# Kernel optimization log

Measured on AMD Instinct MI355X. Metric: run time of the kernel, lower is better.

## Reference

```python
import jax, jax.numpy as jnp
import numpy as np

NEG_BIG = -9.0e15  # matches torch's -9000000000000000.0 mask fill
ALPHA = 0.2        # LeakyReLU negative slope


def setup_inputs() -> dict:
    key = jax.random.key(0)
    k1, k2, k3, k4 = jax.random.split(key, 4)
    bs, N, F_in, F_out = 4, 4096, 512, 64
    x = jax.random.normal(k1, (bs, N, F_in), dtype=jnp.float32)
    adj = jax.random.randint(k2, (N, N), 0, 2, dtype=jnp.int32)
    # xavier_uniform with gain=1.414
    lim_W = 1.414 * np.sqrt(6.0 / (F_in + F_out))
    W = jax.random.uniform(k3, (F_in, F_out), minval=-lim_W, maxval=lim_W, dtype=jnp.float32)
    lim_a = 1.414 * np.sqrt(6.0 / (2 * F_out + 1))
    a = jax.random.uniform(k4, (2 * F_out, 1), minval=-lim_a, maxval=lim_a, dtype=jnp.float32)
    return {"x": x, "adj": adj, "W": W, "a": a}


def reference(x, adj, W, a):
    # h = x @ W : [bs, N, F_out]
    h = jnp.einsum('bnf,fo->bno', x, W)
    F_out = W.shape[1]
    a1, a2 = a[:F_out, 0], a[F_out:, 0]  # each [F_out]
    # e_ij = LeakyReLU(a1.Wh_i + a2.Wh_j) -- same math as the O(N^2*2F) concat
    s1 = jnp.einsum('bno,o->bn', h, a1)  # [bs, N]
    s2 = jnp.einsum('bno,o->bn', h, a2)  # [bs, N]
    e = s1[:, :, None] + s2[:, None, :]  # [bs, N, N]
    e = jax.nn.leaky_relu(e, negative_slope=ALPHA)
    mask = (adj > 0)[None, :, :]
    attention = jnp.where(mask, e, NEG_BIG)
    attention = jax.nn.softmax(attention, axis=-1)
    # dropout is identity in eval mode (p applied only during training)
    h_prime = jnp.einsum('bij,bjo->bio', attention, h)
    return jax.nn.elu(h_prime)  # concat=True path
```

## Files before the change

### kernel.cpp

```cpp
#include <hip/hip_runtime.h>

#define LOG2E 1.4426950408889634f

typedef __attribute__((ext_vector_type(8))) short short8;
typedef __attribute__((ext_vector_type(4))) float f32x4;
using u32 = unsigned int;
using u16 = unsigned short;
using u64 = unsigned long long;

__global__ __launch_bounds__(256) void prep_kernel(const int* __restrict__ adj,
                                                   u32* __restrict__ mask_t,
                                                   const float* __restrict__ W,
                                                   u16* __restrict__ wt) {
    if (blockIdx.x >= 2048) {
        int t = (blockIdx.x - 2048) * 256 + threadIdx.x;
        int n = t >> 7, k4 = (t & 127) << 2;
        u32 c0 = __float_as_uint(W[(size_t)(k4 + 0) * 64 + n]) + 0x8000u;
        u32 c1 = __float_as_uint(W[(size_t)(k4 + 1) * 64 + n]) + 0x8000u;
        u32 c2 = __float_as_uint(W[(size_t)(k4 + 2) * 64 + n]) + 0x8000u;
        u32 c3 = __float_as_uint(W[(size_t)(k4 + 3) * 64 + n]) + 0x8000u;
        uint2 o;
        o.x = (c0 >> 16) | (c1 & 0xffff0000u);
        o.y = (c2 >> 16) | (c3 & 0xffff0000u);
        *(uint2*)(wt + (size_t)n * 512 + k4) = o;
        return;
    }
    const int wid = (blockIdx.x * 256 + threadIdx.x) >> 6;
    const int lane = threadIdx.x & 63;
    for (int t = wid; t < 65536; t += 8192) {
        const int r = t >> 4, c4 = t & 15;
        const int* base = adj + (size_t)r * 4096 + c4 * 256 + lane;
        int v0 = __builtin_nontemporal_load(base);
        int v1 = __builtin_nontemporal_load(base + 64);
        int v2 = __builtin_nontemporal_load(base + 128);
        int v3 = __builtin_nontemporal_load(base + 192);
        u64 b0 = __ballot(v0 > 0);
        u64 b1 = __ballot(v1 > 0);
        u64 b2 = __ballot(v2 > 0);
        u64 b3 = __ballot(v3 > 0);
        if (lane < 8) {
            u64 bv = (lane & 4) ? ((lane & 2) ? b3 : b2) : ((lane & 2) ? b1 : b0);
            u32 w = (u32)(bv >> ((lane & 1) << 5));
            mask_t[(size_t)(c4 * 8 + lane) * 4096 + r] = w;
        }
    }
}

__global__ __launch_bounds__(512) void k1f(const float* __restrict__ x,
                                           const u16* __restrict__ wt,
                                           const float* __restrict__ a,
                                           u16* __restrict__ h_t,
                                           float* __restrict__ s1p,
                                           float* __restrict__ s2p) {
    __shared__ float red[4][16][65];
    const int rt = blockIdx.x, b = blockIdx.y;
    const int tid = threadIdx.x, wave = tid >> 6, lane = tid & 63;
    const int g = wave & 3, kz = wave >> 2;
    const int m = lane & 15, quad = lane >> 4;
    const int row = rt * 64 + g * 16 + m;
    const float* xb = x + ((size_t)b * 4096 + row) * 512 + kz * 256 + quad * 8;
    const u16* wb = wt + (size_t)m * 512 + kz * 256 + quad * 8;

    f32x4 acc[4];
#pragma unroll
    for (int ot = 0; ot < 4; ot++) acc[ot] = (f32x4){0.f, 0.f, 0.f, 0.f};

    union BU { uint4 q; short8 v; };
    float4 ax[2][2];
    BU bw[2][4];
#pragma unroll
    for (int s = 0; s < 2; s++) {
        ax[s][0] = *(const float4*)(xb + s * 32);
        ax[s][1] = *(const float4*)(xb + s * 32 + 4);
#pragma unroll
        for (int ot = 0; ot < 4; ot++)
            bw[s][ot].q = *(const uint4*)(wb + (size_t)ot * 16 * 512 + s * 32);
    }
#pragma unroll
    for (int s = 0; s < 8; s++) {
        const int cur = s & 1;
        union { u32 u[4]; short8 v; } af;
        const float* a0 = (const float*)&ax[cur][0];
#pragma unroll
        for (int p = 0; p < 4; p++) {
            u32 lo = __float_as_uint(a0[2 * p]) + 0x8000u;
            u32 hi = __float_as_uint(a0[2 * p + 1]) + 0x8000u;
            af.u[p] = __builtin_amdgcn_perm(hi, lo, 0x07060302u);
        }
#pragma unroll
        for (int ot = 0; ot < 4; ot++)
            acc[ot] = __builtin_amdgcn_mfma_f32_16x16x32_bf16(af.v, bw[cur][ot].v,
                                                              acc[ot], 0, 0, 0);
        if (s + 2 < 8) {
            ax[cur][0] = *(const float4*)(xb + (s + 2) * 32);
            ax[cur][1] = *(const float4*)(xb + (s + 2) * 32 + 4);
#pragma unroll
            for (int ot = 0; ot < 4; ot++)
                bw[cur][ot].q =
                    *(const uint4*)(wb + (size_t)ot * 16 * 512 + (s + 2) * 32);
        }
    }
    if (kz) {
#pragma unroll
        for (int ot = 0; ot < 4; ot++)
#pragma unroll
            for (int r = 0; r < 4; r++)
                red[g][quad * 4 + r][ot * 16 + m] = acc[ot][r];
    }
    __syncthreads();
    if (kz) return;
#pragma unroll
    for (int ot = 0; ot < 4; ot++)
#pragma unroll
        for (int r = 0; r < 4; r++)
            acc[ot][r] += red[g][quad * 4 + r][ot * 16 + m];

    float a1v[4], a2v[4];
#pragma unroll
    for (int ot = 0; ot < 4; ot++) {
        a1v[ot] = a[ot * 16 + m];
        a2v[ot] = a[64 + ot * 16 + m];
    }
    float s1r[4], s2r[4];
#pragma unroll
    for (int r = 0; r < 4; r++) {
        s1r[r] = 0.f; s2r[r] = 0.f;
#pragma unroll
        for (int ot = 0; ot < 4; ot++) {
            s1r[r] = fmaf(acc[ot][r], a1v[ot], s1r[r]);
            s2r[r] = fmaf(acc[ot][r], a2v[ot], s2r[r]);
        }
    }
#pragma unroll
    for (int d = 1; d < 16; d <<= 1) {
#pragma unroll
        for (int r = 0; r < 4; r++) {
            s1r[r] += __shfl_xor(s1r[r], d);
            s2r[r] += __shfl_xor(s2r[r], d);
        }
    }
    if (m == 0) {
#pragma unroll
        for (int r = 0; r < 4; r++) {
            int rr = rt * 64 + g * 16 + quad * 4 + r;
            s1p[b * 4096 + rr] = s1r[r] * LOG2E;
            s2p[b * 4096 + rr] = s2r[r] * LOG2E;
        }
    }
#pragma unroll
    for (int ot = 0; ot < 4; ot++) {
        u32 b0 = __float_as_uint(acc[ot][0]) + 0x8000u;
        u32 b1 = __float_as_uint(acc[ot][1]) + 0x8000u;
        u32 b2 = __float_as_uint(acc[ot][2]) + 0x8000u;
        u32 b3 = __float_as_uint(acc[ot][3]) + 0x8000u;
        uint2 u;
        u.x = (b0 >> 16) | (b1 & 0xffff0000u);
        u.y = (b2 >> 16) | (b3 & 0xffff0000u);
        *(uint2*)(h_t + ((size_t)(b * 64 + ot * 16 + m)) * 4096
                  + rt * 64 + g * 16 + quad * 4) = u;
    }
}

template <int NSTEP>
__global__ __launch_bounds__(256, 8) void k2_attn(const u16* __restrict__ h_t,
                                                  const u32* __restrict__ mask_t,
                                                  const float* __restrict__ s1p,
                                                  const float* __restrict__ s2p,
                                                  u16* __restrict__ part,
                                                  float* __restrict__ lp) {
    constexpr int JSEG = NSTEP * 32;
    constexpr int T = NSTEP / 2;
    __shared__ u16 hB[2][64 * 64];
    __shared__ float s2l[JSEG];
    const int b = blockIdx.y, seg = blockIdx.z, rb = blockIdx.x;
    const int tid = threadIdx.x, wave = tid >> 6, lane = tid & 63;
    const int m = lane & 15, quad = lane >> 4;
    const int row = rb * 64 + wave * 16 + m;
    const int jstart = seg * JSEG;
    const float t1 = s1p[b * 4096 + row];
    const u16* hsrc = h_t + (size_t)b * 64 * 4096 + jstart;
    const u32* mrow = mask_t + (size_t)(jstart >> 5) * 4096 + row;

    for (int t = tid; t < (JSEG >> 2); t += 256)
        ((float4*)s2l)[t] = ((const float4*)(s2p + b * 4096 + jstart))[t];

    f32x4 acc[4], accd;
#pragma unroll
    for (int ot = 0; ot < 4; ot++) acc[ot] = (f32x4){0.f, 0.f, 0.f, 0.f};
    accd = (f32x4){0.f, 0.f, 0.f, 0.f};

    u32 mw[4];
#pragma unroll
    for (int s = 0; s < 4; s++) mw[s] = mrow[(size_t)s * 4096];
    union { u32 u[4]; short8 v; } ones;
#pragma unroll
    for (int p = 0; p < 4; p++) ones.u[p] = 0x3F803F80u;

    const int cj = tid & 7;
    const int ow = tid >> 3;
    uint4 pf[2];
    pf[0] = *(const uint4*)(hsrc + (size_t)ow * 4096 + (cj << 3));
    pf[1] = *(const uint4*)(hsrc + (size_t)(ow + 32) * 4096 + (cj << 3));
    *(uint4*)(hB[0] + (size_t)ow * 64 + ((cj ^ (ow & 7)) << 3)) = pf[0];
    *(uint4*)(hB[0] + (size_t)(ow + 32) * 64 + ((cj ^ ((ow + 32) & 7)) << 3)) = pf[1];
    __syncthreads();

    for (int jt = 0; jt < T; jt++) {
        const int cb = jt & 1;
        if (jt + 1 < T) {
            pf[0] = *(const uint4*)(hsrc + (size_t)ow * 4096 + (jt + 1) * 64 + (cj << 3));
            pf[1] = *(const uint4*)(hsrc + (size_t)(ow + 32) * 4096 + (jt + 1) * 64 + (cj << 3));
        }
#pragma unroll
        for (int ks = 0; ks < 2; ks++) {
            const int s = jt * 2 + ks;
            const u32 mws = mw[s & 3] >> (quad * 8);
            if (s + 4 < NSTEP) mw[(s + 4) & 3] = mrow[(size_t)(s + 4) * 4096];

            const float4 sa = *(const float4*)&s2l[s * 32 + quad * 8];
            const float4 sb = *(const float4*)&s2l[s * 32 + quad * 8 + 4];
            const float sv[8] = {sa.x, sa.y, sa.z, sa.w, sb.x, sb.y, sb.z, sb.w};
            union { u32 u[4]; short8 v; } af;
#pragma unroll
            for (int p = 0; p < 4; p++) {
                float t0 = t1 + sv[2 * p];
                float u0 = fmaxf(t0, 0.2f * t0);
                float w0 = __builtin_amdgcn_exp2f(u0);
                u32 m0 = (u32)(((int)(mws << (31 - 2 * p))) >> 31);
                u32 w0u = __float_as_uint(w0) & m0;
                float t2 = t1 + sv[2 * p + 1];
                float u2 = fmaxf(t2, 0.2f * t2);
                float w1 = __builtin_amdgcn_exp2f(u2);
                u32 m1 = (u32)(((int)(mws << (30 - 2 * p))) >> 31);
                u32 w1u = __float_as_uint(w1) & m1;
                af.u[p] = __builtin_amdgcn_perm(w1u, w0u, 0x07060302u);
            }
            const int jc = ks * 4 + quad;
#pragma unroll
            for (int ot = 0; ot < 4; ot++) {
                const int o = ot * 16 + m;
                short8 bfv = *(const short8*)(hB[cb] + (size_t)o * 64 + ((jc ^ (o & 7)) << 3));
                acc[ot] = __builtin_amdgcn_mfma_f32_16x16x32_bf16(af.v, bfv, acc[ot], 0, 0, 0);
            }
            accd = __builtin_amdgcn_mfma_f32_16x16x32_bf16(af.v, ones.v, accd, 0, 0, 0);
        }
        if (jt + 1 < T) {
            const int nb = cb ^ 1;
            *(uint4*)(hB[nb] + (size_t)ow * 64 + ((cj ^ (ow & 7)) << 3)) = pf[0];
            *(uint4*)(hB[nb] + (size_t)(ow + 32) * 64 + ((cj ^ ((ow + 32) & 7)) << 3)) = pf[1];
        }
        __syncthreads();
    }
    u16* pb = part + (((size_t)(seg * 4 + b) * 4096) + rb * 64 + wave * 16) * 64;
#pragma unroll
    for (int ot = 0; ot < 4; ot++)
#pragma unroll
        for (int r = 0; r < 4; r++) {
            u32 v = __float_as_uint(acc[ot][r]) + 0x8000u;
            pb[(quad * 4 + r) * 64 + ot * 16 + m] = (u16)(v >> 16);
        }
    if (m == 0) {
        float* lpb = lp + (size_t)(seg * 4 + b) * 4096 + rb * 64 + wave * 16 + quad * 4;
#pragma unroll
        for (int r = 0; r < 4; r++) lpb[r] = accd[r];
    }
}

template <int S>
__global__ __launch_bounds__(256) void k3_fin(const u16* __restrict__ part,
                                              const float* __restrict__ lp,
                                              float* __restrict__ out) {
    int idx = blockIdx.x * 256 + threadIdx.x;
    int o4 = (idx & 15) << 2;
    int bi = idx >> 4;
    uint2 pv[S];
    float lv[S];
#pragma unroll
    for (int s = 0; s < S; s++) {
        pv[s] = *(const uint2*)&part[((size_t)s * 16384 + bi) * 64 + o4];
        lv[s] = lp[(size_t)s * 16384 + bi];
    }
    float p0 = 0.f, p1 = 0.f, p2 = 0.f, p3 = 0.f, l = 0.f;
#pragma unroll
    for (int s = 0; s < S; s++) {
        p0 += __uint_as_float(pv[s].x << 16);
        p1 += __uint_as_float(pv[s].x & 0xffff0000u);
        p2 += __uint_as_float(pv[s].y << 16);
        p3 += __uint_as_float(pv[s].y & 0xffff0000u);
        l += lv[s];
    }
    float rl = 1.f / l;
    p0 *= rl; p1 *= rl; p2 *= rl; p3 *= rl;
    float4 o;
    o.x = p0 > 0.f ? p0 : __builtin_amdgcn_exp2f(p0 * LOG2E) - 1.f;
    o.y = p1 > 0.f ? p1 : __builtin_amdgcn_exp2f(p1 * LOG2E) - 1.f;
    o.z = p2 > 0.f ? p2 : __builtin_amdgcn_exp2f(p2 * LOG2E) - 1.f;
    o.w = p3 > 0.f ? p3 : __builtin_amdgcn_exp2f(p3 * LOG2E) - 1.f;
    *(float4*)&out[(size_t)bi * 64 + o4] = o;
}

extern "C" void kernel_launch(void* const* d_in, const int* in_sizes, int n_in,
                              void* d_out, int out_size, void* d_ws, size_t ws_size,
                              hipStream_t stream) {
    const float* x  = (const float*)d_in[0];
    const int* adj  = (const int*)d_in[1];
    const float* W  = (const float*)d_in[2];
    const float* a  = (const float*)d_in[3];
    float* out = (float*)d_out;
    char* ws = (char*)d_ws;

    u16* h_t   = (u16*)ws;
    u32* maskt = (u32*)(ws + (2 << 20));
    float* s1p = (float*)(ws + (4 << 20));
    float* s2p = s1p + 16384;
    float* lp  = s2p + 16384;
    size_t base = (4u << 20) + 2 * 65536;
    int S = 8;
    while (S > 1 && base + (size_t)S * (65536 + 2097152) + 65536 > ws_size) S >>= 1;
    u16* part = (u16*)(ws + base + (size_t)S * 65536);
    u16* wtp = (u16*)(ws + base + (size_t)S * 65536 + (size_t)S * 2097152);

    prep_kernel<<<2080, 256, 0, stream>>>(adj, maskt, W, wtp);
    k1f<<<dim3(64, 4), 512, 0, stream>>>(x, wtp, a, h_t, s1p, s2p);
    if (S == 8)      k2_attn<16><<<dim3(64, 4, 8), 256, 0, stream>>>(h_t, maskt, s1p, s2p, part, lp);
    else if (S == 4) k2_attn<32><<<dim3(64, 4, 4), 256, 0, stream>>>(h_t, maskt, s1p, s2p, part, lp);
    else if (S == 2) k2_attn<64><<<dim3(64, 4, 2), 256, 0, stream>>>(h_t, maskt, s1p, s2p, part, lp);
    else             k2_attn<128><<<dim3(64, 4, 1), 256, 0, stream>>>(h_t, maskt, s1p, s2p, part, lp);
    if (S == 8)      k3_fin<8><<<1024, 256, 0, stream>>>(part, lp, out);
    else if (S == 4) k3_fin<4><<<1024, 256, 0, stream>>>(part, lp, out);
    else if (S == 2) k3_fin<2><<<1024, 256, 0, stream>>>(part, lp, out);
    else             k3_fin<1><<<1024, 256, 0, stream>>>(part, lp, out);
}
```

Baseline: 160.4 us.

## Fuse prep with projection and finalize into attention via last-block counter

Merges the adjacency-mask packing and the x@W projection into one launch. Each projection block converts W to bf16 itself into swizzled shared memory instead of reading a pre-transposed global copy. Removes the separate finalize kernel: the last attention segment block per row tile, found through an atomic counter, reduces the partials and applies normalization and ELU. This cuts three launches to two and drops the W staging buffer. In exchange every projection block redoes the W conversion, the k0 blocks need 64KB of shared memory, and the fused kernel adds threadfences and an atomic.

```diff
diff --git a/kernel.cpp b/kernel.cpp
--- a/kernel.cpp
+++ b/kernel.cpp
@@ -8,73 +8,76 @@
 using u16 = unsigned short;
 using u64 = unsigned long long;
 
-__global__ __launch_bounds__(256) void prep_kernel(const int* __restrict__ adj,
-                                                   u32* __restrict__ mask_t,
-                                                   const float* __restrict__ W,
-                                                   u16* __restrict__ wt) {
-    if (blockIdx.x >= 2048) {
-        int t = (blockIdx.x - 2048) * 256 + threadIdx.x;
-        int n = t >> 7, k4 = (t & 127) << 2;
-        u32 c0 = __float_as_uint(W[(size_t)(k4 + 0) * 64 + n]) + 0x8000u;
-        u32 c1 = __float_as_uint(W[(size_t)(k4 + 1) * 64 + n]) + 0x8000u;
-        u32 c2 = __float_as_uint(W[(size_t)(k4 + 2) * 64 + n]) + 0x8000u;
-        u32 c3 = __float_as_uint(W[(size_t)(k4 + 3) * 64 + n]) + 0x8000u;
-        uint2 o;
-        o.x = (c0 >> 16) | (c1 & 0xffff0000u);
-        o.y = (c2 >> 16) | (c3 & 0xffff0000u);
-        *(uint2*)(wt + (size_t)n * 512 + k4) = o;
+__global__ __launch_bounds__(512) void k0(const int* __restrict__ adj,
+                                          u32* __restrict__ mask_t,
+                                          const float* __restrict__ x,
+                                          const float* __restrict__ W,
+                                          const float* __restrict__ a,
+                                          u16* __restrict__ h_t,
+                                          float* __restrict__ s1p,
+                                          float* __restrict__ s2p,
+                                          u32* __restrict__ cnt) {
+    __shared__ u16 wtl[64 * 512];
+    const int tid = threadIdx.x;
+
+    if (blockIdx.x < 2048) {
+        if (blockIdx.x == 0 && tid < 256) cnt[tid] = 0;
+        const int wid = (blockIdx.x * 512 + tid) >> 6;
+        const int lane = tid & 63;
+        for (int t = wid; t < 65536; t += 16384) {
+            const int r = t >> 4, c4 = t & 15;
+            const int* base = adj + (size_t)r * 4096 + c4 * 256 + lane;
+            int v0 = __builtin_nontemporal_load(base);
+            int v1 = __builtin_nontemporal_load(base + 64);
+            int v2 = __builtin_nontemporal_load(base + 128);
+            int v3 = __builtin_nontemporal_load(base + 192);
+            u64 b0 = __ballot(v0 > 0);
+            u64 b1 = __ballot(v1 > 0);
+            u64 b2 = __ballot(v2 > 0);
+            u64 b3 = __ballot(v3 > 0);
+            if (lane < 8) {
+                u64 bv = (lane & 4) ? ((lane & 2) ? b3 : b2) : ((lane & 2) ? b1 : b0);
+                u32 w = (u32)(bv >> ((lane & 1) << 5));
+                mask_t[(size_t)(c4 * 8 + lane) * 4096 + r] = w;
+            }
+        }
         return;
     }
-    const int wid = (blockIdx.x * 256 + threadIdx.x) >> 6;
-    const int lane = threadIdx.x & 63;
-    for (int t = wid; t < 65536; t += 8192) {
-        const int r = t >> 4, c4 = t & 15;
-        const int* base = adj + (size_t)r * 4096 + c4 * 256 + lane;
-        int v0 = __builtin_nontemporal_load(base);
-        int v1 = __builtin_nontemporal_load(base + 64);
-        int v2 = __builtin_nontemporal_load(base + 128);
-        int v3 = __builtin_nontemporal_load(base + 192);
-        u64 b0 = __ballot(v0 > 0);
-        u64 b1 = __ballot(v1 > 0);
-        u64 b2 = __ballot(v2 > 0);
-        u64 b3 = __ballot(v3 > 0);
-        if (lane < 8) {
-            u64 bv = (lane & 4) ? ((lane & 2) ? b3 : b2) : ((lane & 2) ? b1 : b0);
-            u32 w = (u32)(bv >> ((lane & 1) << 5));
-            mask_t[(size_t)(c4 * 8 + lane) * 4096 + r] = w;
-        }
-    }
-}
-
-__global__ __launch_bounds__(512) void k1f(const float* __restrict__ x,
-                                           const u16* __restrict__ wt,
-                                           const float* __restrict__ a,
-                                           u16* __restrict__ h_t,
-                                           float* __restrict__ s1p,
-                                           float* __restrict__ s2p) {
-    __shared__ float red[4][16][65];
-    const int rt = blockIdx.x, b = blockIdx.y;
-    const int tid = threadIdx.x, wave = tid >> 6, lane = tid & 63;
+    const int bx = blockIdx.x - 2048;
+    const int rt = bx & 63, b = bx >> 6;
+    {
+        const int kk = tid >> 4, n4 = (tid & 15) << 2;
+#pragma unroll
+        for (int it = 0; it < 16; it++) {
+            int k = kk + it * 32;
+            float4 w4 = *(const float4*)(W + (size_t)k * 64 + n4);
+            const float* wf = (const float*)&w4;
+            int kc = k >> 3, ko = k & 7;
+#pragma unroll
+            for (int i = 0; i < 4; i++) {
+                int n = n4 + i;
+                u32 v = __float_as_uint(wf[i]) + 0x8000u;
+                wtl[n * 512 + ((kc ^ (n & 7)) << 3) + ko] = (u16)(v >> 16);
+            }
+        }
+    }
+    __syncthreads();
+
+    const int wave = tid >> 6, lane = tid & 63;
     const int g = wave & 3, kz = wave >> 2;
     const int m = lane & 15, quad = lane >> 4;
     const int row = rt * 64 + g * 16 + m;
     const float* xb = x + ((size_t)b * 4096 + row) * 512 + kz * 256 + quad * 8;
-    const u16* wb = wt + (size_t)m * 512 + kz * 256 + quad * 8;
 
     f32x4 acc[4];
 #pragma unroll
     for (int ot = 0; ot < 4; ot++) acc[ot] = (f32x4){0.f, 0.f, 0.f, 0.f};
 
-    union BU { uint4 q; short8 v; };
     float4 ax[2][2];
-    BU bw[2][4];
 #pragma unroll
     for (int s = 0; s < 2; s++) {
         ax[s][0] = *(const float4*)(xb + s * 32);
         ax[s][1] = *(const float4*)(xb + s * 32 + 4);
-#pragma unroll
-        for (int ot = 0; ot < 4; ot++)
-            bw[s][ot].q = *(const uint4*)(wb + (size_t)ot * 16 * 512 + s * 32);
     }
 #pragma unroll
     for (int s = 0; s < 8; s++) {
@@ -88,24 +91,25 @@
             af.u[p] = __builtin_amdgcn_perm(hi, lo, 0x07060302u);
         }
 #pragma unroll
-        for (int ot = 0; ot < 4; ot++)
-            acc[ot] = __builtin_amdgcn_mfma_f32_16x16x32_bf16(af.v, bw[cur][ot].v,
-                                                              acc[ot], 0, 0, 0);
+        for (int ot = 0; ot < 4; ot++) {
+            const int n = ot * 16 + m;
+            const int chunk = kz * 32 + s * 4 + quad;
+            short8 bv = *(const short8*)(wtl + n * 512 + ((chunk ^ (n & 7)) << 3));
+            acc[ot] = __builtin_amdgcn_mfma_f32_16x16x32_bf16(af.v, bv, acc[ot], 0, 0, 0);
+        }
         if (s + 2 < 8) {
             ax[cur][0] = *(const float4*)(xb + (s + 2) * 32);
             ax[cur][1] = *(const float4*)(xb + (s + 2) * 32 + 4);
-#pragma unroll
-            for (int ot = 0; ot < 4; ot++)
-                bw[cur][ot].q =
-                    *(const uint4*)(wb + (size_t)ot * 16 * 512 + (s + 2) * 32);
-        }
-    }
+        }
+    }
+    __syncthreads();
+    float* red = (float*)wtl;
     if (kz) {
 #pragma unroll
         for (int ot = 0; ot < 4; ot++)
 #pragma unroll
             for (int r = 0; r < 4; r++)
-                red[g][quad * 4 + r][ot * 16 + m] = acc[ot][r];
+                red[(g * 16 + quad * 4 + r) * 64 + ot * 16 + m] = acc[ot][r];
     }
     __syncthreads();
     if (kz) return;
@@ -113,7 +117,7 @@
     for (int ot = 0; ot < 4; ot++)
 #pragma unroll
         for (int r = 0; r < 4; r++)
-            acc[ot][r] += red[g][quad * 4 + r][ot * 16 + m];
+            acc[ot][r] += red[(g * 16 + quad * 4 + r) * 64 + ot * 16 + m];
 
     float a1v[4], a2v[4];
 #pragma unroll
@@ -167,11 +171,15 @@
                                                   const float* __restrict__ s1p,
                                                   const float* __restrict__ s2p,
                                                   u16* __restrict__ part,
-                                                  float* __restrict__ lp) {
+                                                  float* __restrict__ lp,
+                                                  float* __restrict__ out,
+                                                  u32* __restrict__ cnt) {
     constexpr int JSEG = NSTEP * 32;
+    constexpr int S = 128 / NSTEP;
     constexpr int T = NSTEP / 2;
     __shared__ u16 hB[2][64 * 64];
     __shared__ float s2l[JSEG];
+    __shared__ u32 lastf;
     const int b = blockIdx.y, seg = blockIdx.z, rb = blockIdx.x;
     const int tid = threadIdx.x, wave = tid >> 6, lane = tid & 63;
     const int m = lane & 15, quad = lane >> 4;
@@ -264,39 +272,54 @@
 #pragma unroll
         for (int r = 0; r < 4; r++) lpb[r] = accd[r];
     }
-}
-
-template <int S>
-__global__ __launch_bounds__(256) void k3_fin(const u16* __restrict__ part,
-                                              const float* __restrict__ lp,
-                                              float* __restrict__ out) {
-    int idx = blockIdx.x * 256 + threadIdx.x;
-    int o4 = (idx & 15) << 2;
-    int bi = idx >> 4;
-    uint2 pv[S];
-    float lv[S];
-#pragma unroll
+
+    __threadfence();
+    __syncthreads();
+    if (tid == 0) {
+        u32 old = __hip_atomic_fetch_add(&cnt[b * 64 + rb], 1u,
+                                         __ATOMIC_ACQ_REL, __HIP_MEMORY_SCOPE_AGENT);
+        lastf = (old == S - 1) ? 1u : 0u;
+    }
+    __syncthreads();
+    if (!lastf) return;
+    __threadfence();
+
+    const int frow = tid >> 2, c16 = (tid & 3) << 4;
+    float sums[16];
+#pragma unroll
+    for (int i = 0; i < 16; i++) sums[i] = 0.f;
+    float l = 0.f;
     for (int s = 0; s < S; s++) {
-        pv[s] = *(const uint2*)&part[((size_t)s * 16384 + bi) * 64 + o4];
-        lv[s] = lp[(size_t)s * 16384 + bi];
-    }
-    float p0 = 0.f, p1 = 0.f, p2 = 0.f, p3 = 0.f, l = 0.f;
-#pragma unroll
-    for (int s = 0; s < S; s++) {
-        p0 += __uint_as_float(pv[s].x << 16);
-        p1 += __uint_as_float(pv[s].x & 0xffff0000u);
-        p2 += __uint_as_float(pv[s].y << 16);
-        p3 += __uint_as_float(pv[s].y & 0xffff0000u);
-        l += lv[s];
-    }
-    float rl = 1.f / l;
-    p0 *= rl; p1 *= rl; p2 *= rl; p3 *= rl;
-    float4 o;
-    o.x = p0 > 0.f ? p0 : __builtin_amdgcn_exp2f(p0 * LOG2E) - 1.f;
-    o.y = p1 > 0.f ? p1 : __builtin_amdgcn_exp2f(p1 * LOG2E) - 1.f;
-    o.z = p2 > 0.f ? p2 : __builtin_amdgcn_exp2f(p2 * LOG2E) - 1.f;
-    o.w = p3 > 0.f ? p3 : __builtin_amdgcn_exp2f(p3 * LOG2E) - 1.f;
-    *(float4*)&out[(size_t)bi * 64 + o4] = o;
+        const u16* pp = part + (((size_t)(s * 4 + b) * 4096) + rb * 64 + frow) * 64 + c16;
+        uint4 q0 = *(const uint4*)pp;
+        uint4 q1 = *(const uint4*)(pp + 8);
+        const u32* q = (const u32*)&q0;
+#pragma unroll
+        for (int i = 0; i < 4; i++) {
+            sums[2 * i] += __uint_as_float(q[i] << 16);
+            sums[2 * i + 1] += __uint_as_float(q[i] & 0xffff0000u);
+        }
+        const u32* q2 = (const u32*)&q1;
+#pragma unroll
+        for (int i = 0; i < 4; i++) {
+            sums[8 + 2 * i] += __uint_as_float(q2[i] << 16);
+            sums[9 + 2 * i] += __uint_as_float(q2[i] & 0xffff0000u);
+        }
+        l += lp[(size_t)(s * 4 + b) * 4096 + rb * 64 + frow];
+    }
+    const float rl = 1.f / l;
+    float* ob = out + ((size_t)(b * 4096 + rb * 64 + frow)) * 64 + c16;
+#pragma unroll
+    for (int v4 = 0; v4 < 4; v4++) {
+        float4 o;
+        float* ov = (float*)&o;
+#pragma unroll
+        for (int i = 0; i < 4; i++) {
+            float p = sums[v4 * 4 + i] * rl;
+            ov[i] = p > 0.f ? p : __builtin_amdgcn_exp2f(p * LOG2E) - 1.f;
+        }
+        *(float4*)(ob + v4 * 4) = o;
+    }
 }
 
 extern "C" void kernel_launch(void* const* d_in, const int* in_sizes, int n_in,
@@ -313,21 +336,20 @@
     u32* maskt = (u32*)(ws + (2 << 20));
     float* s1p = (float*)(ws + (4 << 20));
     float* s2p = s1p + 16384;
-    float* lp  = s2p + 16384;
-    size_t base = (4u << 20) + 2 * 65536;
+    u32* cnt   = (u32*)(s2p + 16384);
+    float* lp  = (float*)(ws + (4u << 20) + 2 * 65536 + 1024);
+    size_t base = (4u << 20) + 2 * 65536 + 1024;
     int S = 8;
-    while (S > 1 && base + (size_t)S * (65536 + 2097152) + 65536 > ws_size) S >>= 1;
+    while (S > 1 && base + (size_t)S * (65536 + 2097152) > ws_size) S >>= 1;
     u16* part = (u16*)(ws + base + (size_t)S * 65536);
-    u16* wtp = (u16*)(ws + base + (size_t)S * 65536 + (size_t)S * 2097152);
-
-    prep_kernel<<<2080, 256, 0, stream>>>(adj, maskt, W, wtp);
-    k1f<<<dim3(64, 4), 512, 0, stream>>>(x, wtp, a, h_t, s1p, s2p);
-    if (S == 8)      k2_attn<16><<<dim3(64, 4, 8), 256, 0, stream>>>(h_t, maskt, s1p, s2p, part, lp);
-    else if (S == 4) k2_attn<32><<<dim3(64, 4, 4), 256, 0, stream>>>(h_t, maskt, s1p, s2p, part, lp);
-    else if (S == 2) k2_attn<64><<<dim3(64, 4, 2), 256, 0, stream>>>(h_t, maskt, s1p, s2p, part, lp);
-    else             k2_attn<128><<<dim3(64, 4, 1), 256, 0, stream>>>(h_t, maskt, s1p, s2p, part, lp);
-    if (S == 8)      k3_fin<8><<<1024, 256, 0, stream>>>(part, lp, out);
-    else if (S == 4) k3_fin<4><<<1024, 256, 0, stream>>>(part, lp, out);
-    else if (S == 2) k3_fin<2><<<1024, 256, 0, stream>>>(part, lp, out);
-    else             k3_fin<1><<<1024, 256, 0, stream>>>(part, lp, out);
+
+    k0<<<2304, 512, 0, stream>>>(adj, maskt, x, W, a, h_t, s1p, s2p, cnt);
+    if (S == 8)
+        k2_attn<16><<<dim3(64, 4, 8), 256, 0, stream>>>(h_t, maskt, s1p, s2p, part, lp, out, cnt);
+    else if (S == 4)
+        k2_attn<32><<<dim3(64, 4, 4), 256, 0, stream>>>(h_t, maskt, s1p, s2p, part, lp, out, cnt);
+    else if (S == 2)
+        k2_attn<64><<<dim3(64, 4, 2), 256, 0, stream>>>(h_t, maskt, s1p, s2p, part, lp, out, cnt);
+    else
+        k2_attn<128><<<dim3(64, 4, 1), 256, 0, stream>>>(h_t, maskt, s1p, s2p, part, lp, out, cnt);
 }
```

Result: slower. 484.8 us (+202.3%).

## Fuse mask packing and projection GEMM into one kernel with LDS-staged W

Applied to the files above, without the earlier changes.

Merges the adjacency bit-packing kernel and the x@W projection kernel into a single launch, interleaving projection blocks (every 9th block) among mask-packing blocks so both run concurrently. Each projection block now converts W to bf16 itself into an XOR-swizzled shared-memory tile instead of reading a pre-converted copy from global memory, and the reduction buffer reuses that shared memory. This removes one launch and the serialization between the two phases, but each GEMM block redundantly converts all of W and uses 64KB of LDS, which limits occupancy.

```diff
diff --git a/kernel.cpp b/kernel.cpp
--- a/kernel.cpp
+++ b/kernel.cpp
@@ -8,73 +8,76 @@
 using u16 = unsigned short;
 using u64 = unsigned long long;
 
-__global__ __launch_bounds__(256) void prep_kernel(const int* __restrict__ adj,
-                                                   u32* __restrict__ mask_t,
-                                                   const float* __restrict__ W,
-                                                   u16* __restrict__ wt) {
-    if (blockIdx.x >= 2048) {
-        int t = (blockIdx.x - 2048) * 256 + threadIdx.x;
-        int n = t >> 7, k4 = (t & 127) << 2;
-        u32 c0 = __float_as_uint(W[(size_t)(k4 + 0) * 64 + n]) + 0x8000u;
-        u32 c1 = __float_as_uint(W[(size_t)(k4 + 1) * 64 + n]) + 0x8000u;
-        u32 c2 = __float_as_uint(W[(size_t)(k4 + 2) * 64 + n]) + 0x8000u;
-        u32 c3 = __float_as_uint(W[(size_t)(k4 + 3) * 64 + n]) + 0x8000u;
-        uint2 o;
-        o.x = (c0 >> 16) | (c1 & 0xffff0000u);
-        o.y = (c2 >> 16) | (c3 & 0xffff0000u);
-        *(uint2*)(wt + (size_t)n * 512 + k4) = o;
+__global__ __launch_bounds__(512) void k0(const int* __restrict__ adj,
+                                          u32* __restrict__ mask_t,
+                                          const float* __restrict__ x,
+                                          const float* __restrict__ W,
+                                          const float* __restrict__ a,
+                                          u16* __restrict__ h_t,
+                                          float* __restrict__ s1p,
+                                          float* __restrict__ s2p) {
+    __shared__ u16 wtl[64 * 512];
+    const int tid = threadIdx.x;
+    const int bx = blockIdx.x;
+
+    if (bx % 9 != 0) {
+        const int pidx = bx - 1 - bx / 9;
+        const int wid = (pidx * 512 + tid) >> 6;
+        const int lane = tid & 63;
+        for (int t = wid; t < 65536; t += 16384) {
+            const int r = t >> 4, c4 = t & 15;
+            const int* base = adj + (size_t)r * 4096 + c4 * 256 + lane;
+            int v0 = __builtin_nontemporal_load(base);
+            int v1 = __builtin_nontemporal_load(base + 64);
+            int v2 = __builtin_nontemporal_load(base + 128);
+            int v3 = __builtin_nontemporal_load(base + 192);
+            u64 b0 = __ballot(v0 > 0);
+            u64 b1 = __ballot(v1 > 0);
+            u64 b2 = __ballot(v2 > 0);
+            u64 b3 = __ballot(v3 > 0);
+            if (lane < 8) {
+                u64 bv = (lane & 4) ? ((lane & 2) ? b3 : b2) : ((lane & 2) ? b1 : b0);
+                u32 w = (u32)(bv >> ((lane & 1) << 5));
+                mask_t[(size_t)(c4 * 8 + lane) * 4096 + r] = w;
+            }
+        }
         return;
     }
-    const int wid = (blockIdx.x * 256 + threadIdx.x) >> 6;
-    const int lane = threadIdx.x & 63;
-    for (int t = wid; t < 65536; t += 8192) {
-        const int r = t >> 4, c4 = t & 15;
-        const int* base = adj + (size_t)r * 4096 + c4 * 256 + lane;
-        int v0 = __builtin_nontemporal_load(base);
-        int v1 = __builtin_nontemporal_load(base + 64);
-        int v2 = __builtin_nontemporal_load(base + 128);
-        int v3 = __builtin_nontemporal_load(base + 192);
-        u64 b0 = __ballot(v0 > 0);
-        u64 b1 = __ballot(v1 > 0);
-        u64 b2 = __ballot(v2 > 0);
-        u64 b3 = __ballot(v3 > 0);
-        if (lane < 8) {
-            u64 bv = (lane & 4) ? ((lane & 2) ? b3 : b2) : ((lane & 2) ? b1 : b0);
-            u32 w = (u32)(bv >> ((lane & 1) << 5));
-            mask_t[(size_t)(c4 * 8 + lane) * 4096 + r] = w;
-        }
-    }
-}
-
-__global__ __launch_bounds__(512) void k1f(const float* __restrict__ x,
-                                           const u16* __restrict__ wt,
-                                           const float* __restrict__ a,
-                                           u16* __restrict__ h_t,
-                                           float* __restrict__ s1p,
-                                           float* __restrict__ s2p) {
-    __shared__ float red[4][16][65];
-    const int rt = blockIdx.x, b = blockIdx.y;
-    const int tid = threadIdx.x, wave = tid >> 6, lane = tid & 63;
+    const int kidx = bx / 9;
+    const int rt = kidx & 63, b = kidx >> 6;
+    {
+        const int kk = tid >> 4, n4 = (tid & 15) << 2;
+#pragma unroll
+        for (int it = 0; it < 16; it++) {
+            int k = kk + it * 32;
+            float4 w4 = *(const float4*)(W + (size_t)k * 64 + n4);
+            const float* wf = (const float*)&w4;
+            int kc = k >> 3, ko = k & 7;
+#pragma unroll
+            for (int i = 0; i < 4; i++) {
+                int n = n4 + i;
+                u32 v = __float_as_uint(wf[i]) + 0x8000u;
+                wtl[n * 512 + ((kc ^ (n & 7)) << 3) + ko] = (u16)(v >> 16);
+            }
+        }
+    }
+    __syncthreads();
+
+    const int wave = tid >> 6, lane = tid & 63;
     const int g = wave & 3, kz = wave >> 2;
     const int m = lane & 15, quad = lane >> 4;
     const int row = rt * 64 + g * 16 + m;
     const float* xb = x + ((size_t)b * 4096 + row) * 512 + kz * 256 + quad * 8;
-    const u16* wb = wt + (size_t)m * 512 + kz * 256 + quad * 8;
 
     f32x4 acc[4];
 #pragma unroll
     for (int ot = 0; ot < 4; ot++) acc[ot] = (f32x4){0.f, 0.f, 0.f, 0.f};
 
-    union BU { uint4 q; short8 v; };
     float4 ax[2][2];
-    BU bw[2][4];
 #pragma unroll
     for (int s = 0; s < 2; s++) {
         ax[s][0] = *(const float4*)(xb + s * 32);
         ax[s][1] = *(const float4*)(xb + s * 32 + 4);
-#pragma unroll
-        for (int ot = 0; ot < 4; ot++)
-            bw[s][ot].q = *(const uint4*)(wb + (size_t)ot * 16 * 512 + s * 32);
     }
 #pragma unroll
     for (int s = 0; s < 8; s++) {
@@ -88,24 +91,25 @@
             af.u[p] = __builtin_amdgcn_perm(hi, lo, 0x07060302u);
         }
 #pragma unroll
-        for (int ot = 0; ot < 4; ot++)
-            acc[ot] = __builtin_amdgcn_mfma_f32_16x16x32_bf16(af.v, bw[cur][ot].v,
-                                                              acc[ot], 0, 0, 0);
+        for (int ot = 0; ot < 4; ot++) {
+            const int n = ot * 16 + m;
+            const int chunk = kz * 32 + s * 4 + quad;
+            short8 bv = *(const short8*)(wtl + n * 512 + ((chunk ^ (n & 7)) << 3));
+            acc[ot] = __builtin_amdgcn_mfma_f32_16x16x32_bf16(af.v, bv, acc[ot], 0, 0, 0);
+        }
         if (s + 2 < 8) {
             ax[cur][0] = *(const float4*)(xb + (s + 2) * 32);
             ax[cur][1] = *(const float4*)(xb + (s + 2) * 32 + 4);
-#pragma unroll
-            for (int ot = 0; ot < 4; ot++)
-                bw[cur][ot].q =
-                    *(const uint4*)(wb + (size_t)ot * 16 * 512 + (s + 2) * 32);
-        }
-    }
+        }
+    }
+    __syncthreads();
+    float* red = (float*)wtl;
     if (kz) {
 #pragma unroll
         for (int ot = 0; ot < 4; ot++)
 #pragma unroll
             for (int r = 0; r < 4; r++)
-                red[g][quad * 4 + r][ot * 16 + m] = acc[ot][r];
+                red[(g * 16 + quad * 4 + r) * 64 + ot * 16 + m] = acc[ot][r];
     }
     __syncthreads();
     if (kz) return;
@@ -113,7 +117,7 @@
     for (int ot = 0; ot < 4; ot++)
 #pragma unroll
         for (int r = 0; r < 4; r++)
-            acc[ot][r] += red[g][quad * 4 + r][ot * 16 + m];
+            acc[ot][r] += red[(g * 16 + quad * 4 + r) * 64 + ot * 16 + m];
 
     float a1v[4], a2v[4];
 #pragma unroll
@@ -316,12 +320,10 @@
     float* lp  = s2p + 16384;
     size_t base = (4u << 20) + 2 * 65536;
     int S = 8;
-    while (S > 1 && base + (size_t)S * (65536 + 2097152) + 65536 > ws_size) S >>= 1;
+    while (S > 1 && base + (size_t)S * (65536 + 2097152) > ws_size) S >>= 1;
     u16* part = (u16*)(ws + base + (size_t)S * 65536);
-    u16* wtp = (u16*)(ws + base + (size_t)S * 65536 + (size_t)S * 2097152);
-
-    prep_kernel<<<2080, 256, 0, stream>>>(adj, maskt, W, wtp);
-    k1f<<<dim3(64, 4), 512, 0, stream>>>(x, wtp, a, h_t, s1p, s2p);
+
+    k0<<<2304, 512, 0, stream>>>(adj, maskt, x, W, a, h_t, s1p, s2p);
     if (S == 8)      k2_attn<16><<<dim3(64, 4, 8), 256, 0, stream>>>(h_t, maskt, s1p, s2p, part, lp);
     else if (S == 4) k2_attn<32><<<dim3(64, 4, 4), 256, 0, stream>>>(h_t, maskt, s1p, s2p, part, lp);
     else if (S == 2) k2_attn<64><<<dim3(64, 4, 2), 256, 0, stream>>>(h_t, maskt, s1p, s2p, part, lp);
```

Result: no change. 162.8 us (+1.5%).
